# Kernel optimization log

Measured on AMD Instinct MI355X. Metric: run time of the kernel, lower is better.

Reference implementation:

```python
import jax, jax.numpy as jnp
import numpy as np

DEPTH = 11          # tree depth
D = 1024            # input_width
H = 32              # hidden_width (leaf MLP)
O = 1024            # output_width
B = 4096            # flattened token batch
N_LEAVES = 2 ** DEPTH
N_NODES = 2 ** DEPTH - 1


def setup_inputs() -> dict:
    key = jax.random.key(0)
    ks = jax.random.split(key, 7)
    f1 = 1.0 / np.sqrt(D)
    f2 = 1.0 / np.sqrt(H)
    u = lambda k, shape, f: jax.random.uniform(k, shape, jnp.float32, -f, f)
    return {
        "x": jax.random.normal(ks[0], (B, D), jnp.float32),
        "node_weights": u(ks[1], (N_NODES, D), f1),
        "node_biases": u(ks[2], (N_NODES,), f1),   # (n_nodes,1) in torch; flattened
        "w1s": u(ks[3], (N_LEAVES, D, H), f1),
        "b1s": u(ks[4], (N_LEAVES, H), f1),
        "w2s": u(ks[5], (N_LEAVES, H, O), f2),
        "b2s": u(ks[6], (N_LEAVES, O), f2),
    }


def reference(x, node_weights, node_biases, w1s, b1s, w2s, b2s):
    # --- hard tree descent (eval_forward) ---
    nodes = jnp.zeros((x.shape[0],), jnp.int32)
    for i in range(DEPTH):  # fixed small loop over tree depth
        w = node_weights[nodes]                       # [B, D] gathered plane coeffs
        b = node_biases[nodes]                        # [B]
        score = jnp.einsum('bd,bd->b', x, w) + b      # per-sample dot product
        choice = (score >= 0).astype(jnp.int32)
        platform = 2 ** i - 1
        next_platform = 2 ** (i + 1) - 1
        nodes = (nodes - platform) * 2 + choice + next_platform
    leaves = nodes - (2 ** DEPTH - 1)                 # [B] leaf index per sample

    # --- per-sample leaf MLP with gathered weights ---
    h = jax.nn.relu(jnp.einsum('bd,bdh->bh', x, w1s[leaves]) + b1s[leaves])  # [B, H]
    out = jnp.einsum('bh,bho->bo', h, w2s[leaves]) + b2s[leaves]             # [B, O]
    return out
```

## Files before the change

### kernel.cpp

```cpp
#include <hip/hip_runtime.h>

#define DEPTH 11
#define D 1024
#define H 32
#define OW 1024
#define B 4096
#define N_LEAVES 2048
#define N_NODES 2047
#define SMAX 4
#define MAX_ITEMS 3072

__global__ __launch_bounds__(256) void descent_kernel(
    const float* __restrict__ x, const float* __restrict__ nw,
    const float* __restrict__ nb, int* __restrict__ leaf,
    int* __restrict__ rnk, int* __restrict__ count)
{
    int lane = threadIdx.x & 63;
    int wv   = threadIdx.x >> 6;
    int samp = blockIdx.x * 4 + wv;

    const float4* xp = (const float4*)(x + (size_t)samp * D);
    float4 xf[4];
#pragma unroll
    for (int k = 0; k < 4; k++) xf[k] = xp[lane + 64 * k];

    int node = 0;
#pragma unroll
    for (int i = 0; i < DEPTH; i++) {
        const float4* wp = (const float4*)(nw + (size_t)node * D);
        double s = 0.0;
#pragma unroll
        for (int k = 0; k < 4; k++) {
            float4 wf = wp[lane + 64 * k];
            s += (double)xf[k].x * (double)wf.x;
            s += (double)xf[k].y * (double)wf.y;
            s += (double)xf[k].z * (double)wf.z;
            s += (double)xf[k].w * (double)wf.w;
        }
#pragma unroll
        for (int m = 32; m >= 1; m >>= 1) s += __shfl_xor(s, m, 64);
        double score = s + (double)nb[node];
        int choice = (score >= 0.0) ? 1 : 0;
        node = 2 * node + 1 + choice;
    }
    int lf = node - N_NODES;
    if (lane == 0) {
        leaf[samp] = lf;
        rnk[samp]  = atomicAdd(&count[lf], 1);
    }
}

__global__ __launch_bounds__(256) void scan_kernel(
    const int* __restrict__ count, int* __restrict__ offsets)
{
    __shared__ int tot[256];
    int t = threadIdx.x;
    int c[8], s = 0;
#pragma unroll
    for (int k = 0; k < 8; k++) { c[k] = count[t * 8 + k]; s += c[k]; }
    tot[t] = s;
    __syncthreads();
    for (int off = 1; off < 256; off <<= 1) {
        int v = (t >= off) ? tot[t - off] : 0;
        __syncthreads();
        tot[t] += v;
        __syncthreads();
    }
    int base = (t > 0) ? tot[t - 1] : 0;
#pragma unroll
    for (int k = 0; k < 8; k++) { offsets[t * 8 + k] = base; base += c[k]; }
}

__global__ __launch_bounds__(256) void scatter_kernel(
    const int* __restrict__ leaf, const int* __restrict__ rnk,
    const int* __restrict__ offsets, int* __restrict__ bucket)
{
    int i = blockIdx.x * 256 + threadIdx.x;
    bucket[offsets[leaf[i]] + rnk[i]] = i;
}

__global__ __launch_bounds__(256) void build_items_kernel(
    const int* __restrict__ count, int* __restrict__ items,
    int* __restrict__ nitems)
{
    int l = blockIdx.x * 256 + threadIdx.x;
    int c = count[l];
    if (c > 0) {
        int k = (c + SMAX - 1) / SMAX;
        int base = atomicAdd(nitems, k);
        for (int i = 0; i < k; i++)
            items[base + i] = l | ((i * SMAX) << 11);
    }
}

template <int SS>
__device__ __forceinline__ void mlp_compute(
    int tid, const float* __restrict__ w1, const float* __restrict__ w2,
    const float* __restrict__ b1, const float* __restrict__ b2,
    float (*xs)[D], float (*pl1)[32][SMAX], float (*hs)[H],
    const int* sidx, float* __restrict__ out)
{
    const int lane = tid & 63, wave = tid >> 6;
    const int jq = tid & 7, dg = tid >> 3;
    const float4* w1v = (const float4*)w1;

    float4 acc[SS];
#pragma unroll
    for (int s = 0; s < SS; s++) acc[s] = make_float4(0.f, 0.f, 0.f, 0.f);

#pragma unroll 8
    for (int k = 0; k < 32; k++) {
        int d = dg + (k << 5);
        float4 w = w1v[(d << 3) + jq];
#pragma unroll
        for (int s = 0; s < SS; s++) {
            float xv = xs[s][d];
            acc[s].x += xv * w.x;
            acc[s].y += xv * w.y;
            acc[s].z += xv * w.z;
            acc[s].w += xv * w.w;
        }
    }
#pragma unroll
    for (int m = 8; m <= 32; m <<= 1)
#pragma unroll
        for (int s = 0; s < SS; s++) {
            acc[s].x += __shfl_xor(acc[s].x, m, 64);
            acc[s].y += __shfl_xor(acc[s].y, m, 64);
            acc[s].z += __shfl_xor(acc[s].z, m, 64);
            acc[s].w += __shfl_xor(acc[s].w, m, 64);
        }
    if (lane < 8) {
#pragma unroll
        for (int s = 0; s < SS; s++) {
            pl1[wave][jq * 4 + 0][s] = acc[s].x;
            pl1[wave][jq * 4 + 1][s] = acc[s].y;
            pl1[wave][jq * 4 + 2][s] = acc[s].z;
            pl1[wave][jq * 4 + 3][s] = acc[s].w;
        }
    }
    __syncthreads();
    if (tid < 32 * SS) {
        int s2 = tid >> 5, j2 = tid & 31;
        float sum = pl1[0][j2][s2] + pl1[1][j2][s2] + pl1[2][j2][s2] +
                    pl1[3][j2][s2] + b1[j2];
        hs[s2][j2] = fmaxf(sum, 0.f);
    }
    __syncthreads();

    const float4* w2v = (const float4*)w2;
    float4 o[SS];
#pragma unroll
    for (int s = 0; s < SS; s++) o[s] = make_float4(0.f, 0.f, 0.f, 0.f);
#pragma unroll 8
    for (int jj = 0; jj < H; jj++) {
        float4 w = w2v[(jj << 8) + tid];
#pragma unroll
        for (int s = 0; s < SS; s++) {
            float hv = hs[s][jj];
            o[s].x += hv * w.x;
            o[s].y += hv * w.y;
            o[s].z += hv * w.z;
            o[s].w += hv * w.w;
        }
    }
    float4 bv = ((const float4*)b2)[tid];
#pragma unroll
    for (int s = 0; s < SS; s++) {
        float4 o4;
        o4.x = o[s].x + bv.x;
        o4.y = o[s].y + bv.y;
        o4.z = o[s].z + bv.z;
        o4.w = o[s].w + bv.w;
        ((float4*)(out + (size_t)sidx[s] * OW))[tid] = o4;
    }
}

__global__ __launch_bounds__(256, 8) void mlp_kernel(
    const float* __restrict__ x, const float* __restrict__ w1s,
    const float* __restrict__ b1s, const float* __restrict__ w2s,
    const float* __restrict__ b2s, const int* __restrict__ offsets,
    const int* __restrict__ count, const int* __restrict__ bucket,
    const int* __restrict__ items, const int* __restrict__ nitems,
    float* __restrict__ out)
{
    __shared__ float xs[SMAX][D];
    __shared__ float pl1[4][32][SMAX];
    __shared__ float hs[SMAX][H];
    __shared__ int   sidx[SMAX];

    if ((int)blockIdx.x >= nitems[0]) return;
    int item  = items[blockIdx.x];
    int l     = item & (N_LEAVES - 1);
    int start = item >> 11;
    int S     = min(SMAX, count[l] - start);
    int base  = offsets[l] + start;
    int tid   = threadIdx.x;

    const float* w1 = w1s + (size_t)l * D * H;
    const float* w2 = w2s + (size_t)l * H * OW;
    const float* b1 = b1s + (size_t)l * H;
    const float* b2 = b2s + (size_t)l * OW;

    if (tid < S) sidx[tid] = bucket[base + tid];
    __syncthreads();
    for (int s = 0; s < S; s++) {
        ((float4*)xs[s])[tid] = ((const float4*)(x + (size_t)sidx[s] * D))[tid];
    }
    __syncthreads();
    switch (S) {
        case 1: mlp_compute<1>(tid, w1, w2, b1, b2, xs, pl1, hs, sidx, out); break;
        case 2: mlp_compute<2>(tid, w1, w2, b1, b2, xs, pl1, hs, sidx, out); break;
        case 3: mlp_compute<3>(tid, w1, w2, b1, b2, xs, pl1, hs, sidx, out); break;
        default: mlp_compute<4>(tid, w1, w2, b1, b2, xs, pl1, hs, sidx, out); break;
    }
}

extern "C" void kernel_launch(void* const* d_in, const int* in_sizes, int n_in,
                              void* d_out, int out_size, void* d_ws, size_t ws_size,
                              hipStream_t stream)
{
    const float* x   = (const float*)d_in[0];
    const float* nw  = (const float*)d_in[1];
    const float* nb  = (const float*)d_in[2];
    const float* w1s = (const float*)d_in[3];
    const float* b1s = (const float*)d_in[4];
    const float* w2s = (const float*)d_in[5];
    const float* b2s = (const float*)d_in[6];
    float* out = (float*)d_out;

    int* leaf    = (int*)d_ws;
    int* rnk     = leaf + B;
    int* count   = rnk + B;
    int* offsets = count + N_LEAVES;
    int* bucket  = offsets + N_LEAVES;
    int* items   = bucket + B;
    int* nitems  = items + MAX_ITEMS;

    hipMemsetAsync(count, 0, N_LEAVES * sizeof(int), stream);
    hipMemsetAsync(nitems, 0, sizeof(int), stream);
    descent_kernel<<<B / 4, 256, 0, stream>>>(x, nw, nb, leaf, rnk, count);
    scan_kernel<<<1, 256, 0, stream>>>(count, offsets);
    scatter_kernel<<<B / 256, 256, 0, stream>>>(leaf, rnk, offsets, bucket);
    build_items_kernel<<<N_LEAVES / 256, 256, 0, stream>>>(count, items, nitems);
    mlp_kernel<<<MAX_ITEMS, 256, 0, stream>>>(x, w1s, b1s, w2s, b2s,
                                              offsets, count, bucket,
                                              items, nitems, out);
}
```

Baseline: 143.3 us.

## Double-buffer leaf MLP weights into LDS via async global-to-LDS loads

Stages the leaf's w1 and w2 matrices through a double-buffered LDS tile using global_load_lds, so the next 16KB chunk is prefetched while the current one is computed. The x rows are also loaded directly into LDS asynchronously, and sample indices are kept in registers instead of shared memory. This aims to hide global memory latency in the weight-streaming MLP. In exchange it adds 32KB of LDS per block, extra barriers, and drops the occupancy hint, which may reduce concurrency.

```diff
diff --git a/kernel.cpp b/kernel.cpp
--- a/kernel.cpp
+++ b/kernel.cpp
@@ -9,6 +9,10 @@
 #define N_NODES 2047
 #define SMAX 4
 #define MAX_ITEMS 3072
+#define CHUNKF 4096
+
+typedef __attribute__((address_space(3))) void lds_void;
+typedef const __attribute__((address_space(1))) void glb_void;
 
 __global__ __launch_bounds__(256) void descent_kernel(
     const float* __restrict__ x, const float* __restrict__ nw,
@@ -93,34 +97,66 @@
     }
 }
 
+__device__ __forceinline__ void stage16k(const float* __restrict__ src,
+                                         float* ldsbase, int wave, int lane)
+{
+#pragma unroll
+    for (int i = 0; i < 4; i++) {
+        const float* g = src + wave * 1024 + i * 256 + lane * 4;
+        float*       l = ldsbase + wave * 1024 + i * 256;
+        __builtin_amdgcn_global_load_lds((glb_void*)g, (lds_void*)l, 16, 0, 0);
+    }
+}
+
 template <int SS>
-__device__ __forceinline__ void mlp_compute(
-    int tid, const float* __restrict__ w1, const float* __restrict__ w2,
-    const float* __restrict__ b1, const float* __restrict__ b2,
-    float (*xs)[D], float (*pl1)[32][SMAX], float (*hs)[H],
-    const int* sidx, float* __restrict__ out)
+__device__ __forceinline__ void mlp_item(
+    int tid, const float* __restrict__ x, const float* __restrict__ w1,
+    const float* __restrict__ w2, const float* __restrict__ b1,
+    const float* __restrict__ b2, const int* __restrict__ bucket, int base,
+    float (*xs)[D], float* wbuf, float (*pl1)[32][SMAX], float (*hs)[H],
+    float* __restrict__ out)
 {
     const int lane = tid & 63, wave = tid >> 6;
     const int jq = tid & 7, dg = tid >> 3;
-    const float4* w1v = (const float4*)w1;
+
+    int sid[SS];
+#pragma unroll
+    for (int s = 0; s < SS; s++) sid[s] = bucket[base + s];
+
+#pragma unroll
+    for (int s = 0; s < SS; s++) {
+        const float* g = x + (size_t)sid[s] * D + wave * 256 + lane * 4;
+        float*       l = xs[s] + wave * 256;
+        __builtin_amdgcn_global_load_lds((glb_void*)g, (lds_void*)l, 16, 0, 0);
+    }
+    stage16k(w1, wbuf, wave, lane);
+    __syncthreads();
 
     float4 acc[SS];
 #pragma unroll
     for (int s = 0; s < SS; s++) acc[s] = make_float4(0.f, 0.f, 0.f, 0.f);
 
-#pragma unroll 8
-    for (int k = 0; k < 32; k++) {
-        int d = dg + (k << 5);
-        float4 w = w1v[(d << 3) + jq];
-#pragma unroll
-        for (int s = 0; s < SS; s++) {
-            float xv = xs[s][d];
-            acc[s].x += xv * w.x;
-            acc[s].y += xv * w.y;
-            acc[s].z += xv * w.z;
-            acc[s].w += xv * w.w;
-        }
-    }
+    for (int c = 0; c < 8; c++) {
+        const float* nsrc = (c < 7) ? (w1 + (c + 1) * CHUNKF) : w2;
+        stage16k(nsrc, wbuf + ((c + 1) & 1) * CHUNKF, wave, lane);
+        const float* wb = wbuf + (c & 1) * CHUNKF;
+        int d0 = c * 128;
+#pragma unroll
+        for (int k = 0; k < 4; k++) {
+            int r = dg + (k << 5);
+            float4 w = *(const float4*)(wb + r * 32 + jq * 4);
+#pragma unroll
+            for (int s = 0; s < SS; s++) {
+                float xv = xs[s][d0 + r];
+                acc[s].x += xv * w.x;
+                acc[s].y += xv * w.y;
+                acc[s].z += xv * w.z;
+                acc[s].w += xv * w.w;
+            }
+        }
+        __syncthreads();
+    }
+
 #pragma unroll
     for (int m = 8; m <= 32; m <<= 1)
 #pragma unroll
@@ -148,22 +184,30 @@
     }
     __syncthreads();
 
-    const float4* w2v = (const float4*)w2;
     float4 o[SS];
 #pragma unroll
     for (int s = 0; s < SS; s++) o[s] = make_float4(0.f, 0.f, 0.f, 0.f);
-#pragma unroll 8
-    for (int jj = 0; jj < H; jj++) {
-        float4 w = w2v[(jj << 8) + tid];
-#pragma unroll
-        for (int s = 0; s < SS; s++) {
-            float hv = hs[s][jj];
-            o[s].x += hv * w.x;
-            o[s].y += hv * w.y;
-            o[s].z += hv * w.z;
-            o[s].w += hv * w.w;
-        }
-    }
+
+    for (int c = 0; c < 8; c++) {
+        if (c < 7)
+            stage16k(w2 + (c + 1) * CHUNKF, wbuf + ((c + 1) & 1) * CHUNKF, wave, lane);
+        const float* wb = wbuf + (c & 1) * CHUNKF;
+        int j0 = c * 4;
+#pragma unroll
+        for (int jj = 0; jj < 4; jj++) {
+            float4 w = *(const float4*)(wb + jj * 1024 + tid * 4);
+#pragma unroll
+            for (int s = 0; s < SS; s++) {
+                float hv = hs[s][j0 + jj];
+                o[s].x += hv * w.x;
+                o[s].y += hv * w.y;
+                o[s].z += hv * w.z;
+                o[s].w += hv * w.w;
+            }
+        }
+        __syncthreads();
+    }
+
     float4 bv = ((const float4*)b2)[tid];
 #pragma unroll
     for (int s = 0; s < SS; s++) {
@@ -172,11 +216,11 @@
         o4.y = o[s].y + bv.y;
         o4.z = o[s].z + bv.z;
         o4.w = o[s].w + bv.w;
-        ((float4*)(out + (size_t)sidx[s] * OW))[tid] = o4;
-    }
-}
-
-__global__ __launch_bounds__(256, 8) void mlp_kernel(
+        ((float4*)(out + (size_t)sid[s] * OW))[tid] = o4;
+    }
+}
+
+__global__ __launch_bounds__(256) void mlp_kernel(
     const float* __restrict__ x, const float* __restrict__ w1s,
     const float* __restrict__ b1s, const float* __restrict__ w2s,
     const float* __restrict__ b2s, const int* __restrict__ offsets,
@@ -185,9 +229,9 @@
     float* __restrict__ out)
 {
     __shared__ float xs[SMAX][D];
+    __shared__ float wbuf[2][CHUNKF];
     __shared__ float pl1[4][32][SMAX];
     __shared__ float hs[SMAX][H];
-    __shared__ int   sidx[SMAX];
 
     if ((int)blockIdx.x >= nitems[0]) return;
     int item  = items[blockIdx.x];
@@ -202,17 +246,11 @@
     const float* b1 = b1s + (size_t)l * H;
     const float* b2 = b2s + (size_t)l * OW;
 
-    if (tid < S) sidx[tid] = bucket[base + tid];
-    __syncthreads();
-    for (int s = 0; s < S; s++) {
-        ((float4*)xs[s])[tid] = ((const float4*)(x + (size_t)sidx[s] * D))[tid];
-    }
-    __syncthreads();
     switch (S) {
-        case 1: mlp_compute<1>(tid, w1, w2, b1, b2, xs, pl1, hs, sidx, out); break;
-        case 2: mlp_compute<2>(tid, w1, w2, b1, b2, xs, pl1, hs, sidx, out); break;
-        case 3: mlp_compute<3>(tid, w1, w2, b1, b2, xs, pl1, hs, sidx, out); break;
-        default: mlp_compute<4>(tid, w1, w2, b1, b2, xs, pl1, hs, sidx, out); break;
+        case 1: mlp_item<1>(tid, x, w1, w2, b1, b2, bucket, base, xs, &wbuf[0][0], pl1, hs, out); break;
+        case 2: mlp_item<2>(tid, x, w1, w2, b1, b2, bucket, base, xs, &wbuf[0][0], pl1, hs, out); break;
+        case 3: mlp_item<3>(tid, x, w1, w2, b1, b2, bucket, base, xs, &wbuf[0][0], pl1, hs, out); break;
+        default: mlp_item<4>(tid, x, w1, w2, b1, b2, bucket, base, xs, &wbuf[0][0], pl1, hs, out); break;
     }
 }
 
```

After: 131.8 us. 1.09x faster.
